# Kernel optimization log

Measured on AMD Instinct MI355X. Metric: run time of the kernel, lower is better.

## Reference

```python
import jax, jax.numpy as jnp
import numpy as np

NG, ND = 50000, 20000
EG, ED = 300000, 150000
FG = FD = 256
H = 256
FC = 2048
B = 65536
EPS = 1e-5


def _lrelu(x):
    return jnp.where(x >= 0, x, 0.01 * x)


def _bn(x, g, b):
    # BatchNorm1d in training mode: biased batch stats over the node dim
    m = x.mean(axis=0)
    v = ((x - m) ** 2).mean(axis=0)
    return (x - m) * jax.lax.rsqrt(v + EPS) * g + b


def _gconv(x, edge_index, Wr, br, Ws, n_nodes):
    # PyG GraphConv: out = lin_rel(sum_{j->i} x_j) + lin_root(x_i)
    src, dst = edge_index[0], edge_index[1]
    agg = jax.ops.segment_sum(x[src], dst, num_segments=n_nodes)  # [N, in]
    return agg @ Wr + br + x @ Ws


def setup_inputs() -> dict:
    key = jax.random.key(0)
    ks = iter(jax.random.split(key, 64))
    d = {}
    d["gene_x"] = jax.random.normal(next(ks), (NG, FG), jnp.float32)
    d["disease_x"] = jax.random.normal(next(ks), (ND, FD), jnp.float32)
    d["gene_edge_index"] = jax.random.randint(next(ks), (2, EG), 0, NG, jnp.int32)
    d["disease_edge_index"] = jax.random.randint(next(ks), (2, ED), 0, ND, jnp.int32)
    d["batch_idx"] = jax.random.randint(next(ks), (B, 2), 0, ND, jnp.int32)

    def lin(fin, fout):
        s = 1.0 / np.sqrt(fin)
        W = jax.random.uniform(next(ks), (fin, fout), jnp.float32, -s, s)
        b = jax.random.uniform(next(ks), (fout,), jnp.float32, -s, s)
        return W, b

    for p, fin in (("g", FG), ("d", FD)):
        for i in range(3):
            f = fin if i == 0 else H
            Wr, br = lin(f, H)
            Ws, _ = lin(f, H)
            d[f"{p}{i}_Wr"], d[f"{p}{i}_br"], d[f"{p}{i}_Ws"] = Wr, br, Ws
            d[f"bn{p}{i}_g"] = jnp.ones((H,), jnp.float32)
            d[f"bn{p}{i}_b"] = jnp.zeros((H,), jnp.float32)
    d["lin1_W"], d["lin1_b"] = lin(2 * H, FC)
    d["lin2_W"], d["lin2_b"] = lin(FC, FC // 2)
    d["lin3_W"], d["lin3_b"] = lin(FC // 2, FC // 4)
    d["lin4_W"], d["lin4_b"] = lin(FC // 4, 2)
    return d


def reference(gene_x, disease_x, gene_edge_index, disease_edge_index, batch_idx,
              g0_Wr, g0_br, g0_Ws, g1_Wr, g1_br, g1_Ws, g2_Wr, g2_br, g2_Ws,
              d0_Wr, d0_br, d0_Ws, d1_Wr, d1_br, d1_Ws, d2_Wr, d2_br, d2_Ws,
              bng0_g, bng0_b, bng1_g, bng1_b, bng2_g, bng2_b,
              bnd0_g, bnd0_b, bnd1_g, bnd1_b, bnd2_g, bnd2_b,
              lin1_W, lin1_b, lin2_W, lin2_b, lin3_W, lin3_b, lin4_W, lin4_b):
    # gene tower
    g0 = _bn(_lrelu(_gconv(gene_x, gene_edge_index, g0_Wr, g0_br, g0_Ws, NG)), bng0_g, bng0_b)
    g1 = _bn(_lrelu(_gconv(g0, gene_edge_index, g1_Wr, g1_br, g1_Ws, NG)), bng1_g, bng1_b)
    g2 = _bn(_lrelu(_gconv(g1, gene_edge_index, g2_Wr, g2_br, g2_Ws, NG)), bng2_g, bng2_b)
    gene_out = 0.7 * g0 + 0.2 * g1 + 0.1 * g2
    # disease tower
    h0 = _bn(_lrelu(_gconv(disease_x, disease_edge_index, d0_Wr, d0_br, d0_Ws, ND)), bnd0_g, bnd0_b)
    h1 = _bn(_lrelu(_gconv(h0, disease_edge_index, d1_Wr, d1_br, d1_Ws, ND)), bnd1_g, bnd1_b)
    h2 = _bn(_lrelu(_gconv(h1, disease_edge_index, d2_Wr, d2_br, d2_Ws, ND)), bnd2_g, bnd2_b)
    dis_out = 0.7 * h0 + 0.2 * h1 + 0.1 * h2
    # pair gather + MLP head (dropout is identity in eval)
    x = jnp.concatenate([gene_out[batch_idx[:, 0]], dis_out[batch_idx[:, 1]]], axis=1)
    x = _lrelu(x @ lin1_W + lin1_b)
    x = _lrelu(x @ lin2_W + lin2_b)
    x = _lrelu(x @ lin3_W + lin3_b)
    return x @ lin4_W + lin4_b
```

## Files before the change

### kernel.cpp

```cpp
#include <hip/hip_runtime.h>
#include <hip/hip_bf16.h>
#include <cstdint>
#include <cstddef>

#define N_G 50000
#define N_D 20000
#define E_G 300000
#define E_D 150000
#define BATCH 65536

typedef _Float16 f16;
typedef _Float16 f16x8 __attribute__((ext_vector_type(8)));
typedef _Float16 f16x4 __attribute__((ext_vector_type(4)));
typedef float f32x4 __attribute__((ext_vector_type(4)));

__device__ __forceinline__ float clampf(float v) {
    return fminf(fmaxf(v, -60000.f), 60000.f);
}

__device__ __forceinline__ void gl_lds16(const void* g, void* l) {
    __builtin_amdgcn_global_load_lds(
        (const __attribute__((address_space(1))) unsigned int*)g,
        (__attribute__((address_space(3))) unsigned int*)l, 16, 0, 0);
}

__global__ __launch_bounds__(256) void gemm_f16(
    const f16* __restrict__ A,
    const int* __restrict__ bidx,
    const f16* __restrict__ geneT, const f16* __restrict__ disT, int rowBase,
    const f16* __restrict__ Bt, const float* __restrict__ bias,
    f16* __restrict__ C, int M, int N, int K, int relu, int CB, int RB,
    const float* __restrict__ W4, float* __restrict__ outF)
{
    alignas(16) __shared__ f16 sA[128 * 64];
    alignas(16) __shared__ f16 sB[128 * 64];
    const int t = threadIdx.x;
    const int w = t >> 6, l = t & 63;
    const int wm = w >> 1, wn = w & 1;
    const int q = l >> 4, lr = l & 15;

    int flat = blockIdx.x;
    int cb, rb;
    if ((RB & 7) == 0) {
        int x = flat & 7, idx = flat >> 3;
        int Sx = RB >> 3;
        cb = idx % CB;
        rb = x * Sx + idx / CB;
    } else {
        cb = flat % CB;
        rb = flat / CB;
    }
    const int mBase = rb * 128, nBase = cb * 128;

    const int subrow = l >> 3;
    const int c = l & 7;
    const char* pA[4];
    const char* pD[4];
    const char* pB[4];
    const bool fused = (bidx != nullptr);
    const bool concat = (!fused && disT != nullptr);
    const bool twoSrc = fused || concat;
#pragma unroll
    for (int j = 0; j < 4; j++) {
        int seg = j * 4 + w;
        int lrow = seg * 8 + subrow;
        int coff = ((c ^ (lrow & 7)) << 4);
        if (fused) {
            int rg = rowBase + mBase + lrow;
            int gi = bidx[2 * rg], di = bidx[2 * rg + 1];
            pA[j] = (const char*)geneT + (size_t)gi * 512 + coff;
            pD[j] = (const char*)disT + (size_t)di * 512 + coff;
        } else if (concat) {
            int arow = mBase + lrow; if (arow > M - 1) arow = M - 1;
            pA[j] = (const char*)geneT + (size_t)arow * 512 + coff;
            pD[j] = (const char*)disT + (size_t)arow * 512 + coff;
        } else {
            int arow = mBase + lrow; if (arow > M - 1) arow = M - 1;
            pA[j] = (const char*)A + (size_t)arow * K * 2 + coff;
            pD[j] = nullptr;
        }
        int brow = nBase + lrow; if (brow > N - 1) brow = N - 1;
        pB[j] = (const char*)Bt + (size_t)brow * K * 2 + coff;
    }

    f32x4 acc[4][4] = {};

    for (int k0 = 0; k0 < K; k0 += 64) {
        __syncthreads();
#pragma unroll
        for (int j = 0; j < 4; j++) {
            int seg = j * 4 + w;
            const char* srcA;
            if (twoSrc)
                srcA = (k0 < 256) ? (pA[j] + (size_t)k0 * 2) : (pD[j] + (size_t)(k0 - 256) * 2);
            else
                srcA = pA[j] + (size_t)k0 * 2;
            gl_lds16(srcA, sA + seg * 512);
            gl_lds16(pB[j] + (size_t)k0 * 2, sB + seg * 512);
        }
        __syncthreads();
        f16x8 a0[4], a1[4], b0[4], b1[4];
#pragma unroll
        for (int i = 0; i < 4; i++) {
            int r = wm * 64 + i * 16 + lr;
            int rs = r * 64;
            int x0 = (q ^ (r & 7)) << 3;
            int x1 = ((4 + q) ^ (r & 7)) << 3;
            a0[i] = *(const f16x8*)(sA + rs + x0);
            a1[i] = *(const f16x8*)(sA + rs + x1);
        }
#pragma unroll
        for (int jj = 0; jj < 4; jj++) {
            int r = wn * 64 + jj * 16 + lr;
            int rs = r * 64;
            int x0 = (q ^ (r & 7)) << 3;
            int x1 = ((4 + q) ^ (r & 7)) << 3;
            b0[jj] = *(const f16x8*)(sB + rs + x0);
            b1[jj] = *(const f16x8*)(sB + rs + x1);
        }
#pragma unroll
        for (int i = 0; i < 4; i++)
#pragma unroll
            for (int jj = 0; jj < 4; jj++) {
                acc[i][jj] = __builtin_amdgcn_mfma_f32_16x16x32_f16(a0[i], b0[jj], acc[i][jj], 0, 0, 0);
                acc[i][jj] = __builtin_amdgcn_mfma_f32_16x16x32_f16(a1[i], b1[jj], acc[i][jj], 0, 0, 0);
            }
    }

    if (W4 != nullptr) {
        float w40[4], w41[4];
#pragma unroll
        for (int j = 0; j < 4; j++) {
            int col = nBase + wn * 64 + j * 16 + lr;
            w40[j] = W4[col * 2];
            w41[j] = W4[col * 2 + 1];
        }
#pragma unroll
        for (int i = 0; i < 4; i++) {
#pragma unroll
            for (int r = 0; r < 4; r++) {
                int row = mBase + wm * 64 + i * 16 + q * 4 + r;
                float s0 = 0.f, s1 = 0.f;
#pragma unroll
                for (int j = 0; j < 4; j++) {
                    int col = nBase + wn * 64 + j * 16 + lr;
                    float v = acc[i][j][r] + bias[col];
                    v = v >= 0.f ? v : 0.01f * v;
                    v = clampf(v);
                    s0 += v * w40[j];
                    s1 += v * w41[j];
                }
#pragma unroll
                for (int off = 1; off < 16; off <<= 1) {
                    s0 += __shfl_xor(s0, off);
                    s1 += __shfl_xor(s1, off);
                }
                if (lr == 0 && row < M) {
                    atomicAdd(&outF[(size_t)(rowBase + row) * 2], s0);
                    atomicAdd(&outF[(size_t)(rowBase + row) * 2 + 1], s1);
                }
            }
        }
        return;
    }

    __syncthreads();
    f16* lt = ((w >> 1) ? sB : sA) + (w & 1) * 4096;

    float bj[4];
#pragma unroll
    for (int j = 0; j < 4; j++)
        bj[j] = bias ? bias[nBase + wn * 64 + j * 16 + lr] : 0.f;

#pragma unroll
    for (int i = 0; i < 4; i++)
#pragma unroll
        for (int j = 0; j < 4; j++) {
            int col = j * 16 + lr;
#pragma unroll
            for (int r = 0; r < 4; r++) {
                int row = i * 16 + q * 4 + r;
                float v = acc[i][j][r] + bj[j];
                if (relu) v = v >= 0.f ? v : 0.01f * v;
                v = clampf(v);
                int cs = col ^ ((((row >> 2) & 3) << 4) ^ ((row & 3) << 3));
                lt[row * 64 + cs] = (f16)v;
            }
        }
    __syncthreads();

    const int rr = l >> 3;
    const int c8 = l & 7;
#pragma unroll
    for (int it = 0; it < 8; it++) {
        int row = it * 8 + rr;
        int cs = (c8 * 8) ^ ((((row >> 2) & 3) << 4) ^ ((row & 3) << 3));
        f16x8 vv = *(const f16x8*)(lt + row * 64 + cs);
        int grow = mBase + wm * 64 + row;
        if (grow < M)
            *(f16x8*)(C + (size_t)grow * N + nBase + wn * 64 + c8 * 8) = vv;
    }
}

__global__ __launch_bounds__(512) void gemm256(
    const f16* __restrict__ A,
    const int* __restrict__ bidx,
    const f16* __restrict__ geneT, const f16* __restrict__ disT, int rowBase,
    const f16* __restrict__ Bt, const float* __restrict__ bias,
    f16* __restrict__ C, int M, int N, int K, int relu, int CB, int RB)
{
    alignas(16) __shared__ f16 sm[81920];
    const int t = threadIdx.x;
    const int w = t >> 6, l = t & 63;
    const int wm = w >> 2, wn = w & 3;
    const int q = l >> 4, lr = l & 15;

    int flat = blockIdx.x;
    int cb, rb;
    if ((RB & 7) == 0) {
        int x = flat & 7, idx = flat >> 3;
        int Sx = RB >> 3;
        cb = idx % CB;
        rb = x * Sx + idx / CB;
    } else {
        cb = flat % CB;
        rb = flat / CB;
    }
    const int mBase = rb * 256, nBase = cb * 256;

    const int subrow = l >> 3;
    const int c = l & 7;
    const bool gat = (bidx != nullptr);
    const char* pA[4];
    const char* pD[4];
    const char* pB[4];
#pragma unroll
    for (int jj = 0; jj < 4; jj++) {
        int arow = jj * 64 + w * 8 + subrow;
        int coff = ((c ^ (arow & 7)) << 4);
        if (gat) {
            int rg = rowBase + mBase + arow;
            int gi = bidx[2 * rg], di = bidx[2 * rg + 1];
            pA[jj] = (const char*)geneT + (size_t)gi * 512 + coff;
            pD[jj] = (const char*)disT + (size_t)di * 512 + coff;
        } else {
            int ga = mBase + arow; if (ga > M - 1) ga = M - 1;
            pA[jj] = (const char*)A + (size_t)ga * K * 2 + coff;
            pD[jj] = nullptr;
        }
        int gb = nBase + arow; if (gb > N - 1) gb = N - 1;
        pB[jj] = (const char*)Bt + (size_t)gb * K * 2 + coff;
    }

    f16* const smA = sm;
    f16* const smB = sm + 3 * 16384;

    auto stageA = [&](int abuf, int k0) {
        f16* bA = smA + abuf * 16384;
#pragma unroll
        for (int jj = 0; jj < 4; jj++) {
            int R0 = jj * 64 + w * 8;
            const char* srcA;
            if (gat)
                srcA = (k0 < 256) ? (pA[jj] + (size_t)k0 * 2) : (pD[jj] + (size_t)(k0 - 256) * 2);
            else
                srcA = pA[jj] + (size_t)k0 * 2;
            gl_lds16(srcA, bA + R0 * 64);
        }
    };
    auto stageB = [&](int bbuf, int k0) {
        f16* bB = smB + bbuf * 16384;
#pragma unroll
        for (int jj = 0; jj < 4; jj++) {
            int R0 = jj * 64 + w * 8;
            gl_lds16(pB[jj] + (size_t)k0 * 2, bB + R0 * 64);
        }
    };

    f32x4 acc[8][4] = {};
    const int nkt = K >> 6;

    stageA(0, 0);
    stageB(0, 0);
    if (nkt > 1) stageA(1, 64);

    for (int kt = 0; kt < nkt; kt++) {
        if (kt + 1 < nkt) stageB((kt + 1) & 1, (kt + 1) << 6);
        if (kt + 2 < nkt) stageA((kt + 2) % 3, (kt + 2) << 6);
        if (kt + 2 < nkt)      asm volatile("s_waitcnt vmcnt(12)" ::: "memory");
        else if (kt + 1 < nkt) asm volatile("s_waitcnt vmcnt(8)" ::: "memory");
        else                   asm volatile("s_waitcnt vmcnt(0)" ::: "memory");
        __builtin_amdgcn_s_barrier();
        __builtin_amdgcn_sched_barrier(0);
        const f16* bA = smA + (kt % 3) * 16384;
        const f16* bB = smB + (kt & 1) * 16384;
#pragma unroll
        for (int ks = 0; ks < 2; ks++) {
            f16x8 bf[4];
#pragma unroll
            for (int nf = 0; nf < 4; nf++) {
                int rB = wn * 64 + nf * 16 + lr;
                bf[nf] = *(const f16x8*)(bB + rB * 64 + ((((ks << 2) + q) ^ (rB & 7)) << 3));
            }
#pragma unroll
            for (int mf = 0; mf < 8; mf++) {
                int rA = wm * 128 + mf * 16 + lr;
                f16x8 af = *(const f16x8*)(bA + rA * 64 + ((((ks << 2) + q) ^ (rA & 7)) << 3));
#pragma unroll
                for (int nf = 0; nf < 4; nf++)
                    acc[mf][nf] = __builtin_amdgcn_mfma_f32_16x16x32_f16(af, bf[nf], acc[mf][nf], 0, 0, 0);
            }
        }
        __builtin_amdgcn_sched_barrier(0);
        __builtin_amdgcn_s_barrier();
    }
    __builtin_amdgcn_sched_barrier(0);

    f16* lt = sm + w * 8192;
    float bj[4];
#pragma unroll
    for (int nf = 0; nf < 4; nf++)
        bj[nf] = bias ? bias[nBase + wn * 64 + nf * 16 + lr] : 0.f;

#pragma unroll
    for (int mf = 0; mf < 8; mf++)
#pragma unroll
        for (int nf = 0; nf < 4; nf++) {
            int col = nf * 16 + lr;
#pragma unroll
            for (int r = 0; r < 4; r++) {
                int row = mf * 16 + q * 4 + r;
                float v = acc[mf][nf][r] + bj[nf];
                if (relu) v = v >= 0.f ? v : 0.01f * v;
                v = clampf(v);
                int cs = col ^ ((((row >> 2) & 3) << 4) ^ ((row & 3) << 3));
                lt[row * 64 + cs] = (f16)v;
            }
        }

    const int rr = l >> 3;
    const int c8 = l & 7;
#pragma unroll
    for (int it = 0; it < 16; it++) {
        int row = it * 8 + rr;
        int cs = (c8 * 8) ^ ((((row >> 2) & 3) << 4) ^ ((row & 3) << 3));
        f16x8 vv = *(const f16x8*)(lt + row * 64 + cs);
        int grow = mBase + wm * 128 + row;
        if (grow < M)
            *(f16x8*)(C + (size_t)grow * N + nBase + wn * 64 + c8 * 8) = vv;
    }
}

__global__ __launch_bounds__(256) void gemm_tower(
    const f16* __restrict__ X, const f16* __restrict__ XA,
    const f16* __restrict__ Bt, const float* __restrict__ bias,
    f16* __restrict__ C, int M, int N, int K, int CB, int RB,
    float* __restrict__ stats)
{
    alignas(16) __shared__ f16 sA[128 * 64];
    alignas(16) __shared__ f16 sB[128 * 64];
    const int t = threadIdx.x;
    const int w = t >> 6, l = t & 63;
    const int wm = w >> 1, wn = w & 1;
    const int q = l >> 4, lr = l & 15;

    int flat = blockIdx.x;
    int cb, rb;
    if ((RB & 7) == 0) {
        int x = flat & 7, idx = flat >> 3;
        int Sx = RB >> 3;
        cb = idx % CB;
        rb = x * Sx + idx / CB;
    } else {
        cb = flat % CB;
        rb = flat / CB;
    }
    const int mBase = rb * 128, nBase = cb * 128;

    const int subrow = l >> 3;
    const int c = l & 7;
    const char* pA[4];
    const char* pD[4];
    const char* pB[4];
#pragma unroll
    for (int j = 0; j < 4; j++) {
        int seg = j * 4 + w;
        int lrow = seg * 8 + subrow;
        int coff = ((c ^ (lrow & 7)) << 4);
        int arow = mBase + lrow; if (arow > M - 1) arow = M - 1;
        pA[j] = (const char*)X + (size_t)arow * 512 + coff;
        pD[j] = (const char*)XA + (size_t)arow * 512 + coff;
        int brow = nBase + lrow; if (brow > N - 1) brow = N - 1;
        pB[j] = (const char*)Bt + (size_t)brow * K * 2 + coff;
    }

    f32x4 acc[4][4] = {};

    for (int k0 = 0; k0 < K; k0 += 64) {
        __syncthreads();
#pragma unroll
        for (int j = 0; j < 4; j++) {
            int seg = j * 4 + w;
            const char* srcA = (k0 < 256) ? (pA[j] + (size_t)k0 * 2)
                                          : (pD[j] + (size_t)(k0 - 256) * 2);
            gl_lds16(srcA, sA + seg * 512);
            gl_lds16(pB[j] + (size_t)k0 * 2, sB + seg * 512);
        }
        __syncthreads();
        f16x8 a0[4], a1[4], b0[4], b1[4];
#pragma unroll
        for (int i = 0; i < 4; i++) {
            int r = wm * 64 + i * 16 + lr;
            int rs = r * 64;
            int x0 = (q ^ (r & 7)) << 3;
            int x1 = ((4 + q) ^ (r & 7)) << 3;
            a0[i] = *(const f16x8*)(sA + rs + x0);
            a1[i] = *(const f16x8*)(sA + rs + x1);
        }
#pragma unroll
        for (int jj = 0; jj < 4; jj++) {
            int r = wn * 64 + jj * 16 + lr;
            int rs = r * 64;
            int x0 = (q ^ (r & 7)) << 3;
            int x1 = ((4 + q) ^ (r & 7)) << 3;
            b0[jj] = *(const f16x8*)(sB + rs + x0);
            b1[jj] = *(const f16x8*)(sB + rs + x1);
        }
#pragma unroll
        for (int i = 0; i < 4; i++)
#pragma unroll
            for (int jj = 0; jj < 4; jj++) {
                acc[i][jj] = __builtin_amdgcn_mfma_f32_16x16x32_f16(a0[i], b0[jj], acc[i][jj], 0, 0, 0);
                acc[i][jj] = __builtin_amdgcn_mfma_f32_16x16x32_f16(a1[i], b1[jj], acc[i][jj], 0, 0, 0);
            }
    }

    __syncthreads();
    f16* lt = ((w >> 1) ? sB : sA) + (w & 1) * 4096;

    float bj[4];
#pragma unroll
    for (int j = 0; j < 4; j++)
        bj[j] = bias[nBase + wn * 64 + j * 16 + lr];

    float sj[4] = {0.f, 0.f, 0.f, 0.f}, s2j[4] = {0.f, 0.f, 0.f, 0.f};
#pragma unroll
    for (int i = 0; i < 4; i++)
#pragma unroll
        for (int j = 0; j < 4; j++) {
            int col = j * 16 + lr;
#pragma unroll
            for (int r = 0; r < 4; r++) {
                int row = i * 16 + q * 4 + r;
                float v = acc[i][j][r] + bj[j];
                v = v >= 0.f ? v : 0.01f * v;
                v = clampf(v);
                if ((mBase + wm * 64 + row) < M) { sj[j] += v; s2j[j] += v * v; }
                int cs = col ^ ((((row >> 2) & 3) << 4) ^ ((row & 3) << 3));
                lt[row * 64 + cs] = (f16)v;
            }
        }

#pragma unroll
    for (int j = 0; j < 4; j++) {
        float s = sj[j], s2 = s2j[j];
        s += __shfl_xor(s, 16); s2 += __shfl_xor(s2, 16);
        s += __shfl_xor(s, 32); s2 += __shfl_xor(s2, 32);
        if (q == 0) {
            int col = nBase + wn * 64 + j * 16 + lr;
            if (col < N) {
                atomicAdd(&stats[col], s);
                atomicAdd(&stats[256 + col], s2);
            }
        }
    }
    __syncthreads();

    const int rr = l >> 3;
    const int c8 = l & 7;
#pragma unroll
    for (int it = 0; it < 8; it++) {
        int row = it * 8 + rr;
        int cs = (c8 * 8) ^ ((((row >> 2) & 3) << 4) ^ ((row & 3) << 3));
        f16x8 vv = *(const f16x8*)(lt + row * 64 + cs);
        int grow = mBase + wm * 64 + row;
        if (grow < M)
            *(f16x8*)(C + (size_t)grow * N + nBase + wn * 64 + c8 * 8) = vv;
    }
}

__global__ void cvt_f32_f16(const float* __restrict__ in, f16* __restrict__ out, size_t n) {
    size_t i = ((size_t)blockIdx.x * 256 + threadIdx.x) * 8;
    if (i >= n) return;
    f32x4 a = *(const f32x4*)(in + i);
    f32x4 b = *(const f32x4*)(in + i + 4);
    f16x8 o;
    o[0] = (f16)clampf(a.x); o[1] = (f16)clampf(a.y);
    o[2] = (f16)clampf(a.z); o[3] = (f16)clampf(a.w);
    o[4] = (f16)clampf(b.x); o[5] = (f16)clampf(b.y);
    o[6] = (f16)clampf(b.z); o[7] = (f16)clampf(b.w);
    *(f16x8*)(out + i) = o;
}

__global__ void init_out(const float* __restrict__ b4, float* __restrict__ out, int n) {
    int i = blockIdx.x * 256 + threadIdx.x;
    if (i < n) out[i] = b4[i & 1];
}

__global__ void count_deg(const int* __restrict__ ei, int E, int* __restrict__ deg) {
    int e = blockIdx.x * 256 + threadIdx.x;
    if (e < E) atomicAdd(&deg[ei[E + e]], 1);
}

__global__ void scan_deg(const int* __restrict__ deg, int* __restrict__ rowptr, int Nn) {
    __shared__ int part[1024];
    const int t = threadIdx.x;
    const int C = (Nn + 1023) >> 10;
    const int base = t * C;
    int s = 0;
    for (int i = 0; i < C; i++) { int idx = base + i; if (idx < Nn) s += deg[idx]; }
    part[t] = s;
    __syncthreads();
    for (int off = 1; off < 1024; off <<= 1) {
        int v = (t >= off) ? part[t - off] : 0;
        __syncthreads();
        part[t] += v;
        __syncthreads();
    }
    int pre = (t == 0) ? 0 : part[t - 1];
    for (int i = 0; i < C; i++) {
        int idx = base + i;
        if (idx < Nn) { rowptr[idx] = pre; pre += deg[idx]; }
    }
    if (t == 1023) rowptr[Nn] = part[1023];
}

__global__ void fill_csr(const int* __restrict__ ei, int E, const int* __restrict__ rowptr,
                         int* __restrict__ cursor, int* __restrict__ csr) {
    int e = blockIdx.x * 256 + threadIdx.x;
    if (e < E) {
        int d = ei[E + e];
        int p = rowptr[d] + atomicAdd(&cursor[d], 1);
        csr[p] = ei[e];
    }
}

__global__ void agg_x(const int* __restrict__ rowptr, const int* __restrict__ csr,
                      const f16* __restrict__ X, f16* __restrict__ XA, int Nn) {
    int gid = blockIdx.x * 256 + threadIdx.x;
    int node = gid >> 6, l = gid & 63;
    if (node >= Nn) return;
    int beg = rowptr[node], end = rowptr[node + 1];
    float s0 = 0.f, s1 = 0.f, s2 = 0.f, s3 = 0.f;
    for (int e = beg; e < end; e++) {
        int src = csr[e];
        f16x4 xv = *(const f16x4*)(X + (size_t)src * 256 + l * 4);
        s0 += (float)xv.x; s1 += (float)xv.y; s2 += (float)xv.z; s3 += (float)xv.w;
    }
    f16x4 o;
    o.x = (f16)clampf(s0); o.y = (f16)clampf(s1);
    o.z = (f16)clampf(s2); o.w = (f16)clampf(s3);
    *(f16x4*)(XA + (size_t)node * 256 + l * 4) = o;
}

__global__ void transpose_tile(const float* __restrict__ W, f16* __restrict__ WT,
                               int K, int N, int dstRowOff, int dstColOff, int LK) {
    __shared__ float tile[32][33];
    int n0 = blockIdx.x * 32, k0 = blockIdx.y * 32;
    int tx = threadIdx.x, ty = threadIdx.y;
    for (int yy = ty; yy < 32; yy += 8) {
        int k = k0 + yy, n = n0 + tx;
        tile[yy][tx] = (k < K && n < N) ? W[(size_t)k * N + n] : 0.f;
    }
    __syncthreads();
    for (int yy = ty; yy < 32; yy += 8) {
        int n = n0 + yy, k = k0 + tx;
        if (n < N && k < K)
            WT[(size_t)(dstRowOff + n) * LK + dstColOff + k] = (f16)clampf(tile[tx][yy]);
    }
}

__global__ void transpose_pair(const float* __restrict__ Ws, const float* __restrict__ Wr,
                               f16* __restrict__ WT) {
    __shared__ float tile[32][33];
    const float* W = blockIdx.z ? Wr : Ws;
    const int colOff = blockIdx.z ? 256 : 0;
    int n0 = blockIdx.x * 32, k0 = blockIdx.y * 32;
    int tx = threadIdx.x, ty = threadIdx.y;
    for (int yy = ty; yy < 32; yy += 8)
        tile[yy][tx] = W[(size_t)(k0 + yy) * 256 + n0 + tx];
    __syncthreads();
    for (int yy = ty; yy < 32; yy += 8)
        WT[(size_t)(n0 + yy) * 512 + colOff + k0 + tx] = (f16)clampf(tile[tx][yy]);
}

__global__ void bn_apply(f16* __restrict__ y, const float* __restrict__ stats,
                         const float* __restrict__ g, const float* __restrict__ b,
                         float invN, float w, f16* __restrict__ acc, size_t total,
                         int initAcc) {
    size_t i = ((size_t)blockIdx.x * 256 + threadIdx.x) * 8;
    if (i >= total) return;
    int colb = (int)(i & 255);
    f16x8 yv = *(const f16x8*)(y + i);
    f16x8 av = {};
    if (!initAcc) av = *(const f16x8*)(acc + i);
    f16x8 yo, ao;
#pragma unroll
    for (int j = 0; j < 8; j++) {
        int col = colb + j;
        float m = stats[col] * invN;
        float var = stats[256 + col] * invN - m * m;
        if (var < 0.f) var = 0.f;
        float rs = 1.0f / sqrtf(var + 1e-5f);
        float v = ((float)yv[j] - m) * rs * g[col] + b[col];
        v = clampf(v);
        yo[j] = (f16)v;
        float p = initAcc ? 0.f : (float)av[j];
        ao[j] = (f16)clampf(p + w * v);
    }
    *(f16x8*)(y + i) = yo;
    *(f16x8*)(acc + i) = ao;
}

extern "C" void kernel_launch(void* const* d_in, const int* in_sizes, int n_in,
                              void* d_out, int out_size, void* d_ws, size_t ws_size,
                              hipStream_t stream) {
    char* ws = (char*)d_ws;
    size_t off = 0;
    auto alloc = [&](size_t bytes) -> void* {
        void* p = ws + off;
        off += (bytes + 255) & ~(size_t)255;
        return p;
    };

    f16* gene_out = (f16*)alloc((size_t)N_G * 256 * 2);
    f16* dis_out  = (f16*)alloc((size_t)N_D * 256 * 2);
    f16* W1T = (f16*)alloc((size_t)2048 * 512 * 2);
    f16* W2T = (f16*)alloc((size_t)1024 * 2048 * 2);
    f16* W3T = (f16*)alloc((size_t)512 * 1024 * 2);
    f16* WcatT = (f16*)alloc((size_t)256 * 512 * 2);
    int* csr = (int*)alloc((size_t)E_G * 4);
    int* rowptr = (int*)alloc((size_t)(N_G + 1) * 4);
    int* cnt = (int*)alloc((size_t)N_G * 4);
    float* statsAll = (float*)alloc(6 * 512 * 4);

    char* scratch = ws + off;
    size_t avail = (ws_size > off) ? (ws_size - off) : 0;

    f16* ybA = (f16*)scratch;
    f16* ybB = ybA + (size_t)N_G * 256;
    f16* XAbuf = ybB + (size_t)N_G * 256;

    int R = BATCH;
    while ((size_t)R * 6144 > avail && R > 256) R >>= 1;
    int chunks = BATCH / R;
    f16* h1 = (f16*)scratch;
    f16* h2 = h1 + (size_t)R * 2048;

    const float* gene_x = (const float*)d_in[0];
    const float* disease_x = (const float*)d_in[1];
    const int* g_ei = (const int*)d_in[2];
    const int* d_ei = (const int*)d_in[3];
    const int* bidx = (const int*)d_in[4];
    float* out = (float*)d_out;

    const float wl[3] = {0.7f, 0.2f, 0.1f};

    hipMemsetAsync(statsAll, 0, 6 * 512 * 4, stream);

    auto run_tower = [&](const float* xin, const int* ei, int Nn, int E, int pbase,
                         f16* tout, float* statsBase) {
        size_t nelem = (size_t)Nn * 256;
        int nb8 = (int)((nelem / 8 + 255) / 256);
        cvt_f32_f16<<<nb8, 256, 0, stream>>>(xin, ybA, nelem);
        hipMemsetAsync(cnt, 0, (size_t)Nn * 4, stream);
        count_deg<<<(E + 255) / 256, 256, 0, stream>>>(ei, E, cnt);
        scan_deg<<<1, 1024, 0, stream>>>(cnt, rowptr, Nn);
        hipMemsetAsync(cnt, 0, (size_t)Nn * 4, stream);
        fill_csr<<<(E + 255) / 256, 256, 0, stream>>>(ei, E, rowptr, cnt, csr);
        f16* yin = ybA;
        f16* yout = ybB;
        int RB = (Nn + 127) / 128;
        int RBp = (RB + 7) & ~7;
        for (int l = 0; l < 3; l++) {
            const float* Wr = (const float*)d_in[pbase + l * 5 + 0];
            const float* br = (const float*)d_in[pbase + l * 5 + 1];
            const float* Wss = (const float*)d_in[pbase + l * 5 + 2];
            const float* bg = (const float*)d_in[pbase + l * 5 + 3];
            const float* bb = (const float*)d_in[pbase + l * 5 + 4];
            transpose_pair<<<dim3(8, 8, 2), dim3(32, 8), 0, stream>>>(Wss, Wr, WcatT);
            agg_x<<<(Nn * 64 + 255) / 256, 256, 0, stream>>>(rowptr, csr, yin, XAbuf, Nn);
            float* stats = statsBase + l * 512;
            gemm_tower<<<2 * RBp, 256, 0, stream>>>(yin, XAbuf, WcatT, br, yout,
                                                    Nn, 256, 512, 2, RBp, stats);
            bn_apply<<<nb8, 256, 0, stream>>>(yout, stats, bg, bb, 1.0f / Nn, wl[l],
                                              tout, nelem, l == 0);
            f16* tmp = yin; yin = yout; yout = tmp;
        }
    };

    run_tower(gene_x, g_ei, N_G, E_G, 5, gene_out, statsAll);
    run_tower(disease_x, d_ei, N_D, E_D, 20, dis_out, statsAll + 3 * 512);

    const float* lin1_W = (const float*)d_in[35];
    const float* lin1_b = (const float*)d_in[36];
    const float* lin2_W = (const float*)d_in[37];
    const float* lin2_b = (const float*)d_in[38];
    const float* lin3_W = (const float*)d_in[39];
    const float* lin3_b = (const float*)d_in[40];
    const float* lin4_W = (const float*)d_in[41];
    const float* lin4_b = (const float*)d_in[42];

    transpose_tile<<<dim3(64, 16), dim3(32, 8), 0, stream>>>(lin1_W, W1T, 512, 2048, 0, 0, 512);
    transpose_tile<<<dim3(32, 64), dim3(32, 8), 0, stream>>>(lin2_W, W2T, 2048, 1024, 0, 0, 2048);
    transpose_tile<<<dim3(16, 32), dim3(32, 8), 0, stream>>>(lin3_W, W3T, 1024, 512, 0, 0, 1024);
    init_out<<<(BATCH * 2 + 255) / 256, 256, 0, stream>>>(lin4_b, out, BATCH * 2);

    for (int c = 0; c < chunks; c++) {
        int rb = c * R;
        int RB = R / 128;
        if ((R & 255) == 0) {
            int RB2 = R / 256;
            gemm256<<<8 * RB2, 512, 0, stream>>>(nullptr, bidx, gene_out, dis_out, rb,
                                                 W1T, lin1_b, h1, R, 2048, 512, 1, 8, RB2);
        } else {
            gemm_f16<<<16 * RB, 256, 0, stream>>>(nullptr, bidx, gene_out, dis_out, rb,
                                                  W1T, lin1_b, h1, R, 2048, 512, 1, 16, RB,
                                                  nullptr, nullptr);
        }
        gemm_f16<<<8 * RB, 256, 0, stream>>>(h1, nullptr, nullptr, nullptr, 0,
                                             W2T, lin2_b, h2, R, 1024, 2048, 1, 8, RB,
                                             nullptr, nullptr);
        gemm_f16<<<4 * RB, 256, 0, stream>>>(h2, nullptr, nullptr, nullptr, rb,
                                             W3T, lin3_b, nullptr, R, 512, 1024, 1, 4, RB,
                                             lin4_W, out);
    }
}
```

Before: 1.528 ms.

## Batch gene and disease towers into shared kernel launches

Merges the gene and disease graph towers so each stage (conversion, degree count, scan, CSR fill, aggregation, GEMM, batchnorm apply) runs as one launch that covers both graphs. All six weight transposes are also folded into a single kernel up front. This cuts the number of kernel launches and gives the small disease tower's work more parallelism by sharing a grid with the gene tower. In exchange it needs separate scratch buffers per tower, which uses more workspace memory and may shrink the MLP chunk size.

```diff
diff --git a/kernel.cpp b/kernel.cpp
--- a/kernel.cpp
+++ b/kernel.cpp
@@ -351,11 +351,13 @@
     }
 }
 
-__global__ __launch_bounds__(256) void gemm_tower(
-    const f16* __restrict__ X, const f16* __restrict__ XA,
-    const f16* __restrict__ Bt, const float* __restrict__ bias,
-    f16* __restrict__ C, int M, int N, int K, int CB, int RB,
-    float* __restrict__ stats)
+__global__ __launch_bounds__(256) void gemm_tower2(
+    const f16* __restrict__ Xg, const f16* __restrict__ XAg,
+    const f16* __restrict__ Btg, const float* __restrict__ biasg,
+    f16* __restrict__ Cg, int Mg, int RBg, float* __restrict__ statsg,
+    const f16* __restrict__ Xd, const f16* __restrict__ XAd,
+    const f16* __restrict__ Btd, const float* __restrict__ biasd,
+    f16* __restrict__ Cd, int Md, int RBd, float* __restrict__ statsd)
 {
     alignas(16) __shared__ f16 sA[128 * 64];
     alignas(16) __shared__ f16 sB[128 * 64];
@@ -365,15 +367,25 @@
     const int q = l >> 4, lr = l & 15;
 
     int flat = blockIdx.x;
+    const int geneBlocks = 2 * RBg;
+    const f16* X;  const f16* XA;  const f16* Bt;  const float* bias;
+    f16* C;  int M, RB;  float* stats;
+    if (flat < geneBlocks) {
+        X = Xg; XA = XAg; Bt = Btg; bias = biasg; C = Cg; M = Mg; RB = RBg; stats = statsg;
+    } else {
+        flat -= geneBlocks;
+        X = Xd; XA = XAd; Bt = Btd; bias = biasd; C = Cd; M = Md; RB = RBd; stats = statsd;
+    }
+
     int cb, rb;
     if ((RB & 7) == 0) {
         int x = flat & 7, idx = flat >> 3;
         int Sx = RB >> 3;
-        cb = idx % CB;
-        rb = x * Sx + idx / CB;
+        cb = idx % 2;
+        rb = x * Sx + idx / 2;
     } else {
-        cb = flat % CB;
-        rb = flat / CB;
+        cb = flat % 2;
+        rb = flat / 2;
     }
     const int mBase = rb * 128, nBase = cb * 128;
 
@@ -390,13 +402,13 @@
         int arow = mBase + lrow; if (arow > M - 1) arow = M - 1;
         pA[j] = (const char*)X + (size_t)arow * 512 + coff;
         pD[j] = (const char*)XA + (size_t)arow * 512 + coff;
-        int brow = nBase + lrow; if (brow > N - 1) brow = N - 1;
-        pB[j] = (const char*)Bt + (size_t)brow * K * 2 + coff;
+        int brow = nBase + lrow; if (brow > 255) brow = 255;
+        pB[j] = (const char*)Bt + (size_t)brow * 1024 + coff;
     }
 
     f32x4 acc[4][4] = {};
 
-    for (int k0 = 0; k0 < K; k0 += 64) {
+    for (int k0 = 0; k0 < 512; k0 += 64) {
         __syncthreads();
 #pragma unroll
         for (int j = 0; j < 4; j++) {
@@ -468,10 +480,8 @@
         s += __shfl_xor(s, 32); s2 += __shfl_xor(s2, 32);
         if (q == 0) {
             int col = nBase + wn * 64 + j * 16 + lr;
-            if (col < N) {
-                atomicAdd(&stats[col], s);
-                atomicAdd(&stats[256 + col], s2);
-            }
+            atomicAdd(&stats[col], s);
+            atomicAdd(&stats[256 + col], s2);
         }
     }
     __syncthreads();
@@ -485,21 +495,29 @@
         f16x8 vv = *(const f16x8*)(lt + row * 64 + cs);
         int grow = mBase + wm * 64 + row;
         if (grow < M)
-            *(f16x8*)(C + (size_t)grow * N + nBase + wn * 64 + c8 * 8) = vv;
-    }
-}
-
-__global__ void cvt_f32_f16(const float* __restrict__ in, f16* __restrict__ out, size_t n) {
+            *(f16x8*)(C + (size_t)grow * 256 + nBase + wn * 64 + c8 * 8) = vv;
+    }
+}
+
+__global__ void cvt2(const float* __restrict__ gx, const float* __restrict__ dx,
+                     f16* __restrict__ og, f16* __restrict__ od) {
     size_t i = ((size_t)blockIdx.x * 256 + threadIdx.x) * 8;
-    if (i >= n) return;
-    f32x4 a = *(const f32x4*)(in + i);
-    f32x4 b = *(const f32x4*)(in + i + 4);
+    const size_t ng = (size_t)N_G * 256;
+    const float* in; f16* out;
+    if (i < ng) { in = gx + i; out = og + i; }
+    else {
+        size_t j = i - ng;
+        if (j >= (size_t)N_D * 256) return;
+        in = dx + j; out = od + j;
+    }
+    f32x4 a = *(const f32x4*)in;
+    f32x4 b = *(const f32x4*)(in + 4);
     f16x8 o;
     o[0] = (f16)clampf(a.x); o[1] = (f16)clampf(a.y);
     o[2] = (f16)clampf(a.z); o[3] = (f16)clampf(a.w);
     o[4] = (f16)clampf(b.x); o[5] = (f16)clampf(b.y);
     o[6] = (f16)clampf(b.z); o[7] = (f16)clampf(b.w);
-    *(f16x8*)(out + i) = o;
+    *(f16x8*)out = o;
 }
 
 __global__ void init_out(const float* __restrict__ b4, float* __restrict__ out, int n) {
@@ -507,14 +525,20 @@
     if (i < n) out[i] = b4[i & 1];
 }
 
-__global__ void count_deg(const int* __restrict__ ei, int E, int* __restrict__ deg) {
+__global__ void count_deg2(const int* __restrict__ gei, const int* __restrict__ dei,
+                           int* __restrict__ cntg, int* __restrict__ cntd) {
     int e = blockIdx.x * 256 + threadIdx.x;
-    if (e < E) atomicAdd(&deg[ei[E + e]], 1);
-}
-
-__global__ void scan_deg(const int* __restrict__ deg, int* __restrict__ rowptr, int Nn) {
+    if (e < E_G) atomicAdd(&cntg[gei[E_G + e]], 1);
+    else if (e < E_G + E_D) atomicAdd(&cntd[dei[E_D + (e - E_G)]], 1);
+}
+
+__global__ void scan_deg2(const int* __restrict__ cntg, int* __restrict__ rpg,
+                          const int* __restrict__ cntd, int* __restrict__ rpd) {
     __shared__ int part[1024];
     const int t = threadIdx.x;
+    const int* deg = blockIdx.x ? cntd : cntg;
+    int* rowptr = blockIdx.x ? rpd : rpg;
+    const int Nn = blockIdx.x ? N_D : N_G;
     const int C = (Nn + 1023) >> 10;
     const int base = t * C;
     int s = 0;
@@ -535,21 +559,36 @@
     if (t == 1023) rowptr[Nn] = part[1023];
 }
 
-__global__ void fill_csr(const int* __restrict__ ei, int E, const int* __restrict__ rowptr,
-                         int* __restrict__ cursor, int* __restrict__ csr) {
+__global__ void fill_csr2(const int* __restrict__ gei, const int* __restrict__ dei,
+                          const int* __restrict__ rpg, const int* __restrict__ rpd,
+                          int* __restrict__ curg, int* __restrict__ curd,
+                          int* __restrict__ csrg, int* __restrict__ csrd) {
     int e = blockIdx.x * 256 + threadIdx.x;
-    if (e < E) {
-        int d = ei[E + e];
-        int p = rowptr[d] + atomicAdd(&cursor[d], 1);
-        csr[p] = ei[e];
-    }
-}
-
-__global__ void agg_x(const int* __restrict__ rowptr, const int* __restrict__ csr,
-                      const f16* __restrict__ X, f16* __restrict__ XA, int Nn) {
+    if (e < E_G) {
+        int d = gei[E_G + e];
+        int p = rpg[d] + atomicAdd(&curg[d], 1);
+        csrg[p] = gei[e];
+    } else if (e < E_G + E_D) {
+        int e2 = e - E_G;
+        int d = dei[E_D + e2];
+        int p = rpd[d] + atomicAdd(&curd[d], 1);
+        csrd[p] = dei[e2];
+    }
+}
+
+__global__ void agg_x2(const int* __restrict__ rpg, const int* __restrict__ csrg,
+                       const f16* __restrict__ Xg, f16* __restrict__ XAg,
+                       const int* __restrict__ rpd, const int* __restrict__ csrd,
+                       const f16* __restrict__ Xd, f16* __restrict__ XAd) {
     int gid = blockIdx.x * 256 + threadIdx.x;
     int node = gid >> 6, l = gid & 63;
-    if (node >= Nn) return;
+    const int* rowptr; const int* csr; const f16* X; f16* XA;
+    if (node < N_G) { rowptr = rpg; csr = csrg; X = Xg; XA = XAg; }
+    else {
+        node -= N_G;
+        if (node >= N_D) return;
+        rowptr = rpd; csr = csrd; X = Xd; XA = XAd;
+    }
     int beg = rowptr[node], end = rowptr[node + 1];
     float s0 = 0.f, s1 = 0.f, s2 = 0.f, s3 = 0.f;
     for (int e = beg; e < end; e++) {
@@ -563,47 +602,25 @@
     *(f16x4*)(XA + (size_t)node * 256 + l * 4) = o;
 }
 
-__global__ void transpose_tile(const float* __restrict__ W, f16* __restrict__ WT,
-                               int K, int N, int dstRowOff, int dstColOff, int LK) {
-    __shared__ float tile[32][33];
-    int n0 = blockIdx.x * 32, k0 = blockIdx.y * 32;
-    int tx = threadIdx.x, ty = threadIdx.y;
-    for (int yy = ty; yy < 32; yy += 8) {
-        int k = k0 + yy, n = n0 + tx;
-        tile[yy][tx] = (k < K && n < N) ? W[(size_t)k * N + n] : 0.f;
-    }
-    __syncthreads();
-    for (int yy = ty; yy < 32; yy += 8) {
-        int n = n0 + yy, k = k0 + tx;
-        if (n < N && k < K)
-            WT[(size_t)(dstRowOff + n) * LK + dstColOff + k] = (f16)clampf(tile[tx][yy]);
-    }
-}
-
-__global__ void transpose_pair(const float* __restrict__ Ws, const float* __restrict__ Wr,
-                               f16* __restrict__ WT) {
-    __shared__ float tile[32][33];
-    const float* W = blockIdx.z ? Wr : Ws;
-    const int colOff = blockIdx.z ? 256 : 0;
-    int n0 = blockIdx.x * 32, k0 = blockIdx.y * 32;
-    int tx = threadIdx.x, ty = threadIdx.y;
-    for (int yy = ty; yy < 32; yy += 8)
-        tile[yy][tx] = W[(size_t)(k0 + yy) * 256 + n0 + tx];
-    __syncthreads();
-    for (int yy = ty; yy < 32; yy += 8)
-        WT[(size_t)(n0 + yy) * 512 + colOff + k0 + tx] = (f16)clampf(tile[tx][yy]);
-}
-
-__global__ void bn_apply(f16* __restrict__ y, const float* __restrict__ stats,
-                         const float* __restrict__ g, const float* __restrict__ b,
-                         float invN, float w, f16* __restrict__ acc, size_t total,
-                         int initAcc) {
+__global__ void bn_apply2(f16* __restrict__ yg, f16* __restrict__ yd,
+                          const float* __restrict__ stg, const float* __restrict__ std_,
+                          const float* __restrict__ gg, const float* __restrict__ bg,
+                          const float* __restrict__ gd, const float* __restrict__ bd,
+                          float invNg, float invNd, float wv,
+                          f16* __restrict__ accg, f16* __restrict__ accd, int initAcc) {
     size_t i = ((size_t)blockIdx.x * 256 + threadIdx.x) * 8;
-    if (i >= total) return;
+    const size_t ng = (size_t)N_G * 256;
+    f16* y; f16* acc; const float* stats; const float* g; const float* b; float invN;
+    if (i < ng) { y = yg + i; acc = accg + i; stats = stg; g = gg; b = bg; invN = invNg; }
+    else {
+        size_t j = i - ng;
+        if (j >= (size_t)N_D * 256) return;
+        y = yd + j; acc = accd + j; stats = std_; g = gd; b = bd; invN = invNd;
+    }
     int colb = (int)(i & 255);
-    f16x8 yv = *(const f16x8*)(y + i);
+    f16x8 yv = *(const f16x8*)y;
     f16x8 av = {};
-    if (!initAcc) av = *(const f16x8*)(acc + i);
+    if (!initAcc) av = *(const f16x8*)acc;
     f16x8 yo, ao;
 #pragma unroll
     for (int j = 0; j < 8; j++) {
@@ -616,10 +633,44 @@
         v = clampf(v);
         yo[j] = (f16)v;
         float p = initAcc ? 0.f : (float)av[j];
-        ao[j] = (f16)clampf(p + w * v);
-    }
-    *(f16x8*)(y + i) = yo;
-    *(f16x8*)(acc + i) = ao;
+        ao[j] = (f16)clampf(p + wv * v);
+    }
+    *(f16x8*)y = yo;
+    *(f16x8*)acc = ao;
+}
+
+__global__ void transpose_tile(const float* __restrict__ W, f16* __restrict__ WT,
+                               int K, int N, int dstRowOff, int dstColOff, int LK) {
+    __shared__ float tile[32][33];
+    int n0 = blockIdx.x * 32, k0 = blockIdx.y * 32;
+    int tx = threadIdx.x, ty = threadIdx.y;
+    for (int yy = ty; yy < 32; yy += 8) {
+        int k = k0 + yy, n = n0 + tx;
+        tile[yy][tx] = (k < K && n < N) ? W[(size_t)k * N + n] : 0.f;
+    }
+    __syncthreads();
+    for (int yy = ty; yy < 32; yy += 8) {
+        int n = n0 + yy, k = k0 + tx;
+        if (n < N && k < K)
+            WT[(size_t)(dstRowOff + n) * LK + dstColOff + k] = (f16)clampf(tile[tx][yy]);
+    }
+}
+
+struct WPtrs { const float* p[12]; };
+__global__ void transpose12(WPtrs wp, f16* __restrict__ WT) {
+    __shared__ float tile[32][33];
+    const int z = blockIdx.z;
+    const float* W = wp.p[z];
+    const int s = z >> 1;
+    const int colOff = (z & 1) * 256;
+    f16* dst = WT + (size_t)s * 131072;
+    int n0 = blockIdx.x * 32, k0 = blockIdx.y * 32;
+    int tx = threadIdx.x, ty = threadIdx.y;
+    for (int yy = ty; yy < 32; yy += 8)
+        tile[yy][tx] = W[(size_t)(k0 + yy) * 256 + n0 + tx];
+    __syncthreads();
+    for (int yy = ty; yy < 32; yy += 8)
+        dst[(size_t)(n0 + yy) * 512 + colOff + k0 + tx] = (f16)clampf(tile[tx][yy]);
 }
 
 extern "C" void kernel_launch(void* const* d_in, const int* in_sizes, int n_in,
@@ -638,18 +689,27 @@
     f16* W1T = (f16*)alloc((size_t)2048 * 512 * 2);
     f16* W2T = (f16*)alloc((size_t)1024 * 2048 * 2);
     f16* W3T = (f16*)alloc((size_t)512 * 1024 * 2);
-    f16* WcatT = (f16*)alloc((size_t)256 * 512 * 2);
-    int* csr = (int*)alloc((size_t)E_G * 4);
-    int* rowptr = (int*)alloc((size_t)(N_G + 1) * 4);
-    int* cnt = (int*)alloc((size_t)N_G * 4);
+    f16* WcatT = (f16*)alloc((size_t)6 * 256 * 512 * 2);
+    int* csr_g = (int*)alloc((size_t)E_G * 4);
+    int* csr_d = (int*)alloc((size_t)E_D * 4);
+    int* rp_g = (int*)alloc((size_t)(N_G + 1) * 4);
+    int* rp_d = (int*)alloc((size_t)(N_D + 1) * 4);
+    int* cnt = (int*)alloc((size_t)(N_G + N_D) * 4);
+    int* cnt_g = cnt;
+    int* cnt_d = cnt + N_G;
     float* statsAll = (float*)alloc(6 * 512 * 4);
 
     char* scratch = ws + off;
     size_t avail = (ws_size > off) ? (ws_size - off) : 0;
 
-    f16* ybA = (f16*)scratch;
-    f16* ybB = ybA + (size_t)N_G * 256;
-    f16* XAbuf = ybB + (size_t)N_G * 256;
+    const size_t NSG = (size_t)N_G * 256;
+    const size_t NSD = (size_t)N_D * 256;
+    f16* gX = (f16*)scratch;
+    f16* gY = gX + NSG;
+    f16* gXA = gY + NSG;
+    f16* dX = gXA + NSG;
+    f16* dY = dX + NSD;
+    f16* dXA = dY + NSD;
 
     int R = BATCH;
     while ((size_t)R * 6144 > avail && R > 256) R >>= 1;
@@ -667,40 +727,54 @@
     const float wl[3] = {0.7f, 0.2f, 0.1f};
 
     hipMemsetAsync(statsAll, 0, 6 * 512 * 4, stream);
-
-    auto run_tower = [&](const float* xin, const int* ei, int Nn, int E, int pbase,
-                         f16* tout, float* statsBase) {
-        size_t nelem = (size_t)Nn * 256;
-        int nb8 = (int)((nelem / 8 + 255) / 256);
-        cvt_f32_f16<<<nb8, 256, 0, stream>>>(xin, ybA, nelem);
-        hipMemsetAsync(cnt, 0, (size_t)Nn * 4, stream);
-        count_deg<<<(E + 255) / 256, 256, 0, stream>>>(ei, E, cnt);
-        scan_deg<<<1, 1024, 0, stream>>>(cnt, rowptr, Nn);
-        hipMemsetAsync(cnt, 0, (size_t)Nn * 4, stream);
-        fill_csr<<<(E + 255) / 256, 256, 0, stream>>>(ei, E, rowptr, cnt, csr);
-        f16* yin = ybA;
-        f16* yout = ybB;
-        int RB = (Nn + 127) / 128;
-        int RBp = (RB + 7) & ~7;
+    hipMemsetAsync(cnt, 0, (size_t)(N_G + N_D) * 4, stream);
+    {
+        size_t tot8 = ((NSG + NSD) / 8 + 255) / 256;
+        cvt2<<<(int)tot8, 256, 0, stream>>>(gene_x, disease_x, gX, dX);
+    }
+    count_deg2<<<(E_G + E_D + 255) / 256, 256, 0, stream>>>(g_ei, d_ei, cnt_g, cnt_d);
+    scan_deg2<<<2, 1024, 0, stream>>>(cnt_g, rp_g, cnt_d, rp_d);
+    hipMemsetAsync(cnt, 0, (size_t)(N_G + N_D) * 4, stream);
+    fill_csr2<<<(E_G + E_D + 255) / 256, 256, 0, stream>>>(g_ei, d_ei, rp_g, rp_d,
+                                                           cnt_g, cnt_d, csr_g, csr_d);
+    {
+        WPtrs wp;
         for (int l = 0; l < 3; l++) {
-            const float* Wr = (const float*)d_in[pbase + l * 5 + 0];
-            const float* br = (const float*)d_in[pbase + l * 5 + 1];
-            const float* Wss = (const float*)d_in[pbase + l * 5 + 2];
-            const float* bg = (const float*)d_in[pbase + l * 5 + 3];
-            const float* bb = (const float*)d_in[pbase + l * 5 + 4];
-            transpose_pair<<<dim3(8, 8, 2), dim3(32, 8), 0, stream>>>(Wss, Wr, WcatT);
-            agg_x<<<(Nn * 64 + 255) / 256, 256, 0, stream>>>(rowptr, csr, yin, XAbuf, Nn);
-            float* stats = statsBase + l * 512;
-            gemm_tower<<<2 * RBp, 256, 0, stream>>>(yin, XAbuf, WcatT, br, yout,
-                                                    Nn, 256, 512, 2, RBp, stats);
-            bn_apply<<<nb8, 256, 0, stream>>>(yout, stats, bg, bb, 1.0f / Nn, wl[l],
-                                              tout, nelem, l == 0);
-            f16* tmp = yin; yin = yout; yout = tmp;
-        }
-    };
-
-    run_tower(gene_x, g_ei, N_G, E_G, 5, gene_out, statsAll);
-    run_tower(disease_x, d_ei, N_D, E_D, 20, dis_out, statsAll + 3 * 512);
+            wp.p[l * 2 + 0] = (const float*)d_in[5 + l * 5 + 2];
+            wp.p[l * 2 + 1] = (const float*)d_in[5 + l * 5 + 0];
+            wp.p[6 + l * 2 + 0] = (const float*)d_in[20 + l * 5 + 2];
+            wp.p[6 + l * 2 + 1] = (const float*)d_in[20 + l * 5 + 0];
+        }
+        transpose12<<<dim3(8, 8, 12), dim3(32, 8), 0, stream>>>(wp, WcatT);
+    }
+
+    const int RBg = ((N_G + 127) / 128 + 7) & ~7;
+    const int RBd = ((N_D + 127) / 128 + 7) & ~7;
+    f16* gIn = gX; f16* gOut = gY;
+    f16* dIn = dX; f16* dOut = dY;
+    int aggBlocks = ((N_G + N_D) * 64 + 255) / 256;
+    int bnBlocks = (int)(((NSG + NSD) / 8 + 255) / 256);
+    for (int l = 0; l < 3; l++) {
+        const float* br_g = (const float*)d_in[5 + l * 5 + 1];
+        const float* bg_g = (const float*)d_in[5 + l * 5 + 3];
+        const float* bb_g = (const float*)d_in[5 + l * 5 + 4];
+        const float* br_d = (const float*)d_in[20 + l * 5 + 1];
+        const float* bg_d = (const float*)d_in[20 + l * 5 + 3];
+        const float* bb_d = (const float*)d_in[20 + l * 5 + 4];
+        agg_x2<<<aggBlocks, 256, 0, stream>>>(rp_g, csr_g, gIn, gXA,
+                                              rp_d, csr_d, dIn, dXA);
+        gemm_tower2<<<2 * RBg + 2 * RBd, 256, 0, stream>>>(
+            gIn, gXA, WcatT + (size_t)l * 131072, br_g, gOut, N_G, RBg, statsAll + l * 512,
+            dIn, dXA, WcatT + (size_t)(3 + l) * 131072, br_d, dOut, N_D, RBd,
+            statsAll + (3 + l) * 512);
+        bn_apply2<<<bnBlocks, 256, 0, stream>>>(gOut, dOut,
+                                                statsAll + l * 512, statsAll + (3 + l) * 512,
+                                                bg_g, bb_g, bg_d, bb_d,
+                                                1.0f / N_G, 1.0f / N_D, wl[l],
+                                                gene_out, dis_out, l == 0);
+        f16* tmp = gIn; gIn = gOut; gOut = tmp;
+        tmp = dIn; dIn = dOut; dOut = tmp;
+    }
 
     const float* lin1_W = (const float*)d_in[35];
     const float* lin1_b = (const float*)d_in[36];
```

After: 1.328 ms. 1.15x faster.
